# Optimization experiments

Measured on AMD Instinct MI355X. Metric: run time of the kernel, lower is better.

Reference implementation:

```python
import jax, jax.numpy as jnp
import numpy as np

IN_FEATURES = 16080
TREES = 64
LEAVES = 128
CLASSES = 16
BATCH = 64


def setup_inputs() -> dict:
    key = jax.random.key(0)
    k_x, k_w, k_b, k_c = jax.random.split(key, 4)
    x = jax.random.normal(k_x, (BATCH, TREES, IN_FEATURES), dtype=jnp.float32)
    # nn.Linear(16080, leaves): weight [leaves, in], bias [leaves]
    lim = 1.0 / np.sqrt(IN_FEATURES)
    W = jax.random.uniform(k_w, (LEAVES, IN_FEATURES), minval=-lim, maxval=lim, dtype=jnp.float32)
    b = jax.random.uniform(k_b, (LEAVES,), minval=-lim, maxval=lim, dtype=jnp.float32)
    # contribution parameter ~ U(-1, 1), shape [trees, leaves, classes]
    contribution = jax.random.uniform(k_c, (TREES, LEAVES, CLASSES), minval=-1.0, maxval=1.0, dtype=jnp.float32)
    return {"x": x, "W": W, "b": b, "contribution": contribution}


def reference(x, W, b, contribution):
    # Linear + Hardtanh: [B, T, L]
    symbolic_paths = jnp.clip(jnp.einsum('bti,li->btl', x, W) + b, -1.0, 1.0)
    # Fused form of the per-(tree,leaf) outer-product loop: [B, T, L, C]
    class_value = symbolic_paths[..., None] * contribution[None]
    p = jax.nn.softmax(class_value, axis=-1)
    # 1 - sum(p^2) over classes (Gini-style impurity): [B, T, L]
    class_value = jnp.sum(1.0 - p * p, axis=-1)
    return (symbolic_paths, class_value)
```

## Files before the change

### kernel.cpp

```cpp
#include <hip/hip_runtime.h>
#include <hip/hip_bf16.h>
#include <stdint.h>

#define IN_F   16080
#define NTREES 64
#define NLEAF  128
#define NCLS   16
#define NBATCH 64
#define M_TOT  (NBATCH*NTREES)
#define OUT_HALF (M_TOT*NLEAF)

#define BM 64
#define BN 128
#define BK 64
#define KSPLIT 16
#define NSTEPS ((IN_F + BK - 1)/BK)
#define LDS_STRIDE 72

typedef __attribute__((ext_vector_type(8))) short short8;
typedef __attribute__((ext_vector_type(4))) float f32x4;

__device__ __forceinline__ uint32_t pack_bf16x2(float lo, float hi){
  uint32_t a = __builtin_bit_cast(uint32_t, lo);
  uint32_t b = __builtin_bit_cast(uint32_t, hi);
  a = (a + 0x7fffu + ((a >> 16) & 1u)) >> 16;
  b = (b + 0x7fffu + ((b >> 16) & 1u)) & 0xffff0000u;
  return a | b;
}

__global__ __launch_bounds__(256, 4)
void gemm_split_kernel(const float* __restrict__ X,
                       const float* __restrict__ Wg,
                       float* __restrict__ accbuf){
  __shared__ __align__(16) uint16_t As[BM * LDS_STRIDE];
  __shared__ __align__(16) uint16_t Bs[BN * LDS_STRIDE];

  const int tid = threadIdx.x;
  const int m0  = blockIdx.x * BM;
  const int kc  = blockIdx.y;
  const int s0  = (kc * NSTEPS) / KSPLIT;
  const int s1  = ((kc + 1) * NSTEPS) / KSPLIT;

  const int lane = tid & 63;
  const int wv   = tid >> 6;
  const int fr   = lane & 15;
  const int fq   = lane >> 4;

  f32x4 acc[8];
  #pragma unroll
  for (int i = 0; i < 8; ++i) acc[i] = (f32x4){0.f, 0.f, 0.f, 0.f};

  for (int s = s0; s < s1; ++s){
    const int k0 = s * BK;
    __syncthreads();

    #pragma unroll
    for (int j = 0; j < 4; ++j){
      int lin = tid + j * 256;
      int r   = lin >> 4;
      int c4  = (lin & 15) << 2;
      int gk  = k0 + c4;
      float x0 = 0.f, x1 = 0.f, x2 = 0.f, x3 = 0.f;
      if (gk + 4 <= IN_F){
        float4 v = *(const float4*)(X + (size_t)(m0 + r) * IN_F + gk);
        x0 = v.x; x1 = v.y; x2 = v.z; x3 = v.w;
      }
      *(uint2*)&As[r * LDS_STRIDE + c4] =
          make_uint2(pack_bf16x2(x0, x1), pack_bf16x2(x2, x3));
    }
    #pragma unroll
    for (int j = 0; j < 8; ++j){
      int lin = tid + j * 256;
      int r   = lin >> 4;
      int c4  = (lin & 15) << 2;
      int gk  = k0 + c4;
      float x0 = 0.f, x1 = 0.f, x2 = 0.f, x3 = 0.f;
      if (gk + 4 <= IN_F){
        float4 v = *(const float4*)(Wg + (size_t)r * IN_F + gk);
        x0 = v.x; x1 = v.y; x2 = v.z; x3 = v.w;
      }
      *(uint2*)&Bs[r * LDS_STRIDE + c4] =
          make_uint2(pack_bf16x2(x0, x1), pack_bf16x2(x2, x3));
    }
    __syncthreads();

    short8 a0 = *(const short8*)&As[(wv * 16 + fr) * LDS_STRIDE + fq * 8];
    short8 a1 = *(const short8*)&As[(wv * 16 + fr) * LDS_STRIDE + 32 + fq * 8];
    #pragma unroll
    for (int nt = 0; nt < 8; ++nt){
      short8 b0 = *(const short8*)&Bs[(nt * 16 + fr) * LDS_STRIDE + fq * 8];
      acc[nt] = __builtin_amdgcn_mfma_f32_16x16x32_bf16(a0, b0, acc[nt], 0, 0, 0);
    }
    #pragma unroll
    for (int nt = 0; nt < 8; ++nt){
      short8 b1 = *(const short8*)&Bs[(nt * 16 + fr) * LDS_STRIDE + 32 + fq * 8];
      acc[nt] = __builtin_amdgcn_mfma_f32_16x16x32_bf16(a1, b1, acc[nt], 0, 0, 0);
    }
  }

  const int rbase = m0 + wv * 16 + fq * 4;
  #pragma unroll
  for (int nt = 0; nt < 8; ++nt){
    int col = nt * 16 + fr;
    #pragma unroll
    for (int r = 0; r < 4; ++r){
      atomicAdd(&accbuf[(size_t)(rbase + r) * NLEAF + col], acc[nt][r]);
    }
  }
}

__global__ __launch_bounds__(256)
void epilogue_kernel(float* __restrict__ out,
                     const float* __restrict__ bias,
                     const float* __restrict__ contrib){
  int idx = blockIdx.x * 256 + threadIdx.x;
  int l   = idx & (NLEAF - 1);
  int row = idx >> 7;
  int t   = row & (NTREES - 1);

  float s = out[idx] + bias[l];
  s = fminf(1.f, fmaxf(-1.f, s));
  out[idx] = s;

  const float4* cp = (const float4*)(contrib + (((size_t)t * NLEAF + l) << 4));
  float4 c0 = cp[0], c1 = cp[1], c2 = cp[2], c3 = cp[3];
  float v[16] = { s*c0.x, s*c0.y, s*c0.z, s*c0.w,
                  s*c1.x, s*c1.y, s*c1.z, s*c1.w,
                  s*c2.x, s*c2.y, s*c2.z, s*c2.w,
                  s*c3.x, s*c3.y, s*c3.z, s*c3.w };
  float m = v[0];
  #pragma unroll
  for (int c = 1; c < 16; ++c) m = fmaxf(m, v[c]);
  float se = 0.f, se2 = 0.f;
  #pragma unroll
  for (int c = 0; c < 16; ++c){
    float e = __expf(v[c] - m);
    se  += e;
    se2 += e * e;
  }
  out[OUT_HALF + idx] = (float)NCLS - se2 / (se * se);
}

extern "C" void kernel_launch(void* const* d_in, const int* in_sizes, int n_in,
                              void* d_out, int out_size, void* d_ws, size_t ws_size,
                              hipStream_t stream){
  const float* X       = (const float*)d_in[0];
  const float* Wg      = (const float*)d_in[1];
  const float* bias    = (const float*)d_in[2];
  const float* contrib = (const float*)d_in[3];
  float* out = (float*)d_out;

  hipMemsetAsync(out, 0, (size_t)OUT_HALF * sizeof(float), stream);

  dim3 g1(M_TOT / BM, KSPLIT);
  gemm_split_kernel<<<g1, 256, 0, stream>>>(X, Wg, out);

  epilogue_kernel<<<OUT_HALF / 256, 256, 0, stream>>>(out, bias, contrib);
}
```

Measured before the change: 444.0 us.

## Load W directly to LDS as fp32 with swizzle; keep X fragments in registers

The X tile now goes straight from global memory into registers in MFMA fragment layout, so it is no longer staged through LDS. The W tile is copied into LDS as fp32 using global_load_lds DMA with an XOR swizzle, and out-of-range reads are pointed at a zeroed workspace page. Conversion to bf16 happens at fragment-read time, and the wave tiling changes to 2x2 so each B fragment feeds two MFMAs. This aims to remove VGPR round trips and LDS write traffic, at the cost of twice the LDS footprint and redundant per-wave conversion of B.

```diff
diff --git a/kernel.cpp b/kernel.cpp
--- a/kernel.cpp
+++ b/kernel.cpp
@@ -15,25 +15,28 @@
 #define BK 64
 #define KSPLIT 16
 #define NSTEPS ((IN_F + BK - 1)/BK)
-#define LDS_STRIDE 72
 
 typedef __attribute__((ext_vector_type(8))) short short8;
 typedef __attribute__((ext_vector_type(4))) float f32x4;
 
-__device__ __forceinline__ uint32_t pack_bf16x2(float lo, float hi){
-  uint32_t a = __builtin_bit_cast(uint32_t, lo);
-  uint32_t b = __builtin_bit_cast(uint32_t, hi);
-  a = (a + 0x7fffu + ((a >> 16) & 1u)) >> 16;
-  b = (b + 0x7fffu + ((b >> 16) & 1u)) & 0xffff0000u;
-  return a | b;
+typedef const __attribute__((address_space(1))) uint32_t gu32_t;
+typedef __attribute__((address_space(3))) uint32_t su32_t;
+
+__device__ __forceinline__ short8 cvt8(float4 lo, float4 hi){
+  union { short8 s8; __hip_bfloat162 h2[4]; } u;
+  u.h2[0] = __float22bfloat162_rn(make_float2(lo.x, lo.y));
+  u.h2[1] = __float22bfloat162_rn(make_float2(lo.z, lo.w));
+  u.h2[2] = __float22bfloat162_rn(make_float2(hi.x, hi.y));
+  u.h2[3] = __float22bfloat162_rn(make_float2(hi.z, hi.w));
+  return u.s8;
 }
 
 __global__ __launch_bounds__(256, 4)
 void gemm_split_kernel(const float* __restrict__ X,
                        const float* __restrict__ Wg,
-                       float* __restrict__ accbuf){
-  __shared__ __align__(16) uint16_t As[BM * LDS_STRIDE];
-  __shared__ __align__(16) uint16_t Bs[BN * LDS_STRIDE];
+                       float* __restrict__ accbuf,
+                       const float* __restrict__ zeropage){
+  __shared__ __align__(16) float BsF[BN * BK];
 
   const int tid = threadIdx.x;
   const int m0  = blockIdx.x * BM;
@@ -43,68 +46,85 @@
 
   const int lane = tid & 63;
   const int wv   = tid >> 6;
+  const int wm   = wv & 1;
+  const int wn   = wv >> 1;
   const int fr   = lane & 15;
   const int fq   = lane >> 4;
 
-  f32x4 acc[8];
+  f32x4 acc[2][4];
   #pragma unroll
-  for (int i = 0; i < 8; ++i) acc[i] = (f32x4){0.f, 0.f, 0.f, 0.f};
+  for (int mt = 0; mt < 2; ++mt)
+    #pragma unroll
+    for (int nt = 0; nt < 4; ++nt) acc[mt][nt] = (f32x4){0.f,0.f,0.f,0.f};
 
   for (int s = s0; s < s1; ++s){
     const int k0 = s * BK;
     __syncthreads();
 
+    float4 av[2][2][2];
     #pragma unroll
-    for (int j = 0; j < 4; ++j){
-      int lin = tid + j * 256;
-      int r   = lin >> 4;
-      int c4  = (lin & 15) << 2;
-      int gk  = k0 + c4;
-      float x0 = 0.f, x1 = 0.f, x2 = 0.f, x3 = 0.f;
-      if (gk + 4 <= IN_F){
-        float4 v = *(const float4*)(X + (size_t)(m0 + r) * IN_F + gk);
-        x0 = v.x; x1 = v.y; x2 = v.z; x3 = v.w;
-      }
-      *(uint2*)&As[r * LDS_STRIDE + c4] =
-          make_uint2(pack_bf16x2(x0, x1), pack_bf16x2(x2, x3));
+    for (int mt = 0; mt < 2; ++mt){
+      const float* rowp = X + (size_t)(m0 + wm*32 + mt*16 + fr) * IN_F;
+      #pragma unroll
+      for (int h = 0; h < 2; ++h)
+        #pragma unroll
+        for (int q = 0; q < 2; ++q){
+          int gk = k0 + h*32 + fq*8 + q*4;
+          av[mt][h][q] = (gk + 4 <= IN_F) ? *(const float4*)(rowp + gk)
+                                          : make_float4(0.f,0.f,0.f,0.f);
+        }
     }
+
     #pragma unroll
     for (int j = 0; j < 8; ++j){
-      int lin = tid + j * 256;
+      int lin = j*256 + tid;
       int r   = lin >> 4;
-      int c4  = (lin & 15) << 2;
-      int gk  = k0 + c4;
-      float x0 = 0.f, x1 = 0.f, x2 = 0.f, x3 = 0.f;
-      if (gk + 4 <= IN_F){
-        float4 v = *(const float4*)(Wg + (size_t)r * IN_F + gk);
-        x0 = v.x; x1 = v.y; x2 = v.z; x3 = v.w;
-      }
-      *(uint2*)&Bs[r * LDS_STRIDE + c4] =
-          make_uint2(pack_bf16x2(x0, x1), pack_bf16x2(x2, x3));
+      int p   = lin & 15;
+      int c   = p ^ (r & 7);
+      int gk  = k0 + c*4;
+      const float* gp = (gk + 4 <= IN_F) ? (Wg + (size_t)r * IN_F + gk)
+                                         : zeropage;
+      __builtin_amdgcn_global_load_lds((gu32_t*)gp, (su32_t*)(BsF + lin*4),
+                                       16, 0, 0);
     }
+
+    short8 af[2][2];
+    #pragma unroll
+    for (int mt = 0; mt < 2; ++mt)
+      #pragma unroll
+      for (int h = 0; h < 2; ++h)
+        af[mt][h] = cvt8(av[mt][h][0], av[mt][h][1]);
+
     __syncthreads();
 
-    short8 a0 = *(const short8*)&As[(wv * 16 + fr) * LDS_STRIDE + fq * 8];
-    short8 a1 = *(const short8*)&As[(wv * 16 + fr) * LDS_STRIDE + 32 + fq * 8];
     #pragma unroll
-    for (int nt = 0; nt < 8; ++nt){
-      short8 b0 = *(const short8*)&Bs[(nt * 16 + fr) * LDS_STRIDE + fq * 8];
-      acc[nt] = __builtin_amdgcn_mfma_f32_16x16x32_bf16(a0, b0, acc[nt], 0, 0, 0);
-    }
-    #pragma unroll
-    for (int nt = 0; nt < 8; ++nt){
-      short8 b1 = *(const short8*)&Bs[(nt * 16 + fr) * LDS_STRIDE + 32 + fq * 8];
-      acc[nt] = __builtin_amdgcn_mfma_f32_16x16x32_bf16(a1, b1, acc[nt], 0, 0, 0);
+    for (int nt = 0; nt < 4; ++nt){
+      const int l  = wn*64 + nt*16 + fr;
+      const int xw = l & 7;
+      const float* rowb = BsF + l*64;
+      #pragma unroll
+      for (int h = 0; h < 2; ++h){
+        int c0 = h*8 + fq*2;
+        float4 b0 = *(const float4*)(rowb + ((c0    ) ^ xw)*4);
+        float4 b1 = *(const float4*)(rowb + ((c0 + 1) ^ xw)*4);
+        short8 bf = cvt8(b0, b1);
+        #pragma unroll
+        for (int mt = 0; mt < 2; ++mt)
+          acc[mt][nt] = __builtin_amdgcn_mfma_f32_16x16x32_bf16(
+                            af[mt][h], bf, acc[mt][nt], 0, 0, 0);
+      }
     }
   }
 
-  const int rbase = m0 + wv * 16 + fq * 4;
   #pragma unroll
-  for (int nt = 0; nt < 8; ++nt){
-    int col = nt * 16 + fr;
+  for (int mt = 0; mt < 2; ++mt){
+    const int rbase = m0 + wm*32 + mt*16 + fq*4;
     #pragma unroll
-    for (int r = 0; r < 4; ++r){
-      atomicAdd(&accbuf[(size_t)(rbase + r) * NLEAF + col], acc[nt][r]);
+    for (int nt = 0; nt < 4; ++nt){
+      int col = wn*64 + nt*16 + fr;
+      #pragma unroll
+      for (int r = 0; r < 4; ++r)
+        atomicAdd(&accbuf[(size_t)(rbase + r) * NLEAF + col], acc[mt][nt][r]);
     }
   }
 }
@@ -151,9 +171,10 @@
   float* out = (float*)d_out;
 
   hipMemsetAsync(out, 0, (size_t)OUT_HALF * sizeof(float), stream);
+  hipMemsetAsync(d_ws, 0, 256, stream);
 
   dim3 g1(M_TOT / BM, KSPLIT);
-  gemm_split_kernel<<<g1, 256, 0, stream>>>(X, Wg, out);
+  gemm_split_kernel<<<g1, 256, 0, stream>>>(X, Wg, out, (const float*)d_ws);
 
   epilogue_kernel<<<OUT_HALF / 256, 256, 0, stream>>>(out, bias, contrib);
 }
```

New measurement: 429.0 us. 3.4% less time.
